# Optimization experiments

Hardware: AMD Instinct MI355X
Metric: run time of the kernel (lower is better)

## Reference

```python
import jax, jax.numpy as jnp
import numpy as np

KERNEL = 3

def setup_inputs() -> dict:
    key = jax.random.key(0)
    k1, k2 = jax.random.split(key)
    x = jax.random.normal(k1, (32, 64, 64, 64), dtype=jnp.float32)
    weights = jax.random.normal(k2, (128, 64, KERNEL * KERNEL), dtype=jnp.float32)
    return {"x": x, "weights": weights}

def reference(x, weights):
    # x: (B, C, H, W); weights: (OC, C, k*k) with torch-unfold ordering
    # (channel slowest, kernel row-major) -> reshape to OIHW conv kernel.
    B, C, H, W = x.shape
    OC = weights.shape[0]
    wk = weights.reshape(OC, C, KERNEL, KERNEL)
    # stride-1, dilation-1, VALID conv == the unfold + per-(oc,c) matmul sum
    y = jax.lax.conv_general_dilated(
        x, wk, window_strides=(1, 1), padding="VALID",
        dimension_numbers=("NCHW", "OIHW", "NCHW"))
    Ho, Wo = y.shape[2], y.shape[3]
    # Faithful replication of the original's layout bug: results are laid out
    # as [oc*B + b] then reinterpreted via view(B, OC, Ho, Wo).
    y = jnp.transpose(y, (1, 0, 2, 3)).reshape(B, OC, Ho, Wo)
    return y
```

## Files before the change

kernel.cpp:

```cpp
#include <hip/hip_runtime.h>


typedef __attribute__((ext_vector_type(8))) short short8;
typedef __attribute__((ext_vector_type(4))) float f32x4;
typedef __attribute__((ext_vector_type(4))) unsigned int uint4v;

__device__ __forceinline__ unsigned short f2bf(float f) {
    unsigned u = __builtin_bit_cast(unsigned, f);
    u = (u + 0x7FFFu + ((u >> 16) & 1u)) >> 16;
    return (unsigned short)u;
}

__device__ __forceinline__ void glds16(const void* g, void* s) {
    __builtin_amdgcn_global_load_lds(
        (const __attribute__((address_space(1))) unsigned int*)g,
        (__attribute__((address_space(3))) unsigned int*)s, 16, 0, 0);
}

__global__ __launch_bounds__(256)
void transpose_x(const float* __restrict__ x, char* __restrict__ xT) {
    __shared__ float tile[64][65];
    const int tid = threadIdx.x;
    const int h = blockIdx.x, b = blockIdx.y;

    #pragma unroll
    for (int i = 0; i < 4; ++i) {
        const int idx = i * 256 + tid;
        const int c = idx >> 4, j = idx & 15;
        const float4 v = *(const float4*)(x + (size_t)(((b * 64 + c) * 64 + h) * 64 + j * 4));
        tile[c][j * 4 + 0] = v.x; tile[c][j * 4 + 1] = v.y;
        tile[c][j * 4 + 2] = v.z; tile[c][j * 4 + 3] = v.w;
    }
    __syncthreads();

    #pragma unroll
    for (int i = 0; i < 2; ++i) {
        const int idx = i * 256 + tid;
        const int col = idx >> 3, q = idx & 7;
        unsigned int wds[4];
        #pragma unroll
        for (int jj = 0; jj < 4; ++jj) {
            const unsigned short lo = f2bf(tile[q * 8 + 2 * jj + 0][col]);
            const unsigned short hi = f2bf(tile[q * 8 + 2 * jj + 1][col]);
            wds[jj] = (unsigned)lo | ((unsigned)hi << 16);
        }
        uint4v v; v[0] = wds[0]; v[1] = wds[1]; v[2] = wds[2]; v[3] = wds[3];
        *(uint4v*)(xT + (size_t)(((b * 64 + h) * 64 + col) * 128) + ((q ^ (col & 7)) * 16)) = v;
    }
}

__global__ __launch_bounds__(256)
void pack_w(const float* __restrict__ w, char* __restrict__ wT) {
    const int id = blockIdx.x * 256 + threadIdx.x;
    const int t = id >> 10;
    const int rem = id & 1023;
    const int oc = rem >> 3, q = rem & 7;
    unsigned int wds[4];
    #pragma unroll
    for (int jj = 0; jj < 4; ++jj) {
        const unsigned short lo = f2bf(w[(size_t)oc * 576 + (q * 8 + 2 * jj + 0) * 9 + t]);
        const unsigned short hi = f2bf(w[(size_t)oc * 576 + (q * 8 + 2 * jj + 1) * 9 + t]);
        wds[jj] = (unsigned)lo | ((unsigned)hi << 16);
    }
    uint4v v; v[0] = wds[0]; v[1] = wds[1]; v[2] = wds[2]; v[3] = wds[3];
    *(uint4v*)(wT + (size_t)(t * 16384 + oc * 128) + ((q ^ (oc & 7)) * 16)) = v;
}

__global__ __launch_bounds__(256, 2)
void quanv_mfma(const char* __restrict__ xT, const char* __restrict__ wT,
                float* __restrict__ out) {
    __shared__ __align__(16) char lds[65536];
    char* sx = lds;
    char* sw = lds + 49152;

    const int tid = threadIdx.x;
    const int lane = tid & 63;
    const int wid = tid >> 6;
    const int hot = blockIdx.x;
    const int b   = blockIdx.y;
    const int ho0 = hot * 4;

    for (int k = wid; k < 48; k += 4) {
        const int r = k >> 3, sub = k & 7;
        int gr = ho0 + r; if (gr > 63) gr = 63;
        glds16(xT + (size_t)((b * 64 + gr) * 8192 + sub * 1024 + lane * 16),
               sx + k * 1024);
    }
    for (int k = wid; k < 16; k += 4)
        glds16(wT + (size_t)(k * 1024 + lane * 16), sw + k * 1024);
    __syncthreads();

    const int l15 = lane & 15;
    const int quad = lane >> 4;
    const int r = wid;
    const int ho = ho0 + r;

    f32x4 acc[8][4];
    #pragma unroll
    for (int mt = 0; mt < 8; ++mt)
        #pragma unroll
        for (int nt = 0; nt < 4; ++nt)
            acc[mt][nt] = (f32x4){0.f, 0.f, 0.f, 0.f};

    #pragma unroll
    for (int tap = 0; tap < 9; ++tap) {
        const int kh = tap / 3, kw = tap % 3;

        uint4v pf[4];
        if (tap < 8) {
            #pragma unroll
            for (int i = 0; i < 4; ++i)
                pf[i] = *(const uint4v*)(wT + (size_t)((tap + 1) * 16384 +
                                                      (wid * 4 + i) * 1024 + lane * 16));
        }

        #pragma unroll
        for (int s = 0; s < 2; ++s) {
            const int q = s * 4 + quad;
            short8 a[8], bf[4];
            const int abase = l15 * 128 + ((q ^ (l15 & 7)) * 16);
            #pragma unroll
            for (int mt = 0; mt < 8; ++mt)
                a[mt] = *(const short8*)(sw + abase + mt * 2048);
            const int cb = kw + l15;
            const int bbase = (r + kh) * 8192 + cb * 128 + ((q ^ (cb & 7)) * 16);
            #pragma unroll
            for (int nt = 0; nt < 4; ++nt)
                bf[nt] = *(const short8*)(sx + bbase + nt * 2048);
            #pragma unroll
            for (int mt = 0; mt < 8; ++mt)
                #pragma unroll
                for (int nt = 0; nt < 4; ++nt)
                    acc[mt][nt] = __builtin_amdgcn_mfma_f32_16x16x32_bf16(
                        a[mt], bf[nt], acc[mt][nt], 0, 0, 0);
        }

        if (tap < 8) {
            __syncthreads();
            #pragma unroll
            for (int i = 0; i < 4; ++i)
                *(uint4v*)(sw + (wid * 4 + i) * 1024 + lane * 16) = pf[i];
            __syncthreads();
        }
    }

    if (ho < 62) {
        #pragma unroll
        for (int mt = 0; mt < 8; ++mt) {
            #pragma unroll
            for (int i = 0; i < 4; ++i) {
                const int oc = mt * 16 + quad * 4 + i;
                float* op = out + ((size_t)(oc * 32 + b) * 62 + ho) * 62;
                #pragma unroll
                for (int nt = 0; nt < 4; ++nt) {
                    const int wo = nt * 16 + l15;
                    if (wo < 62) op[wo] = acc[mt][nt][i];
                }
            }
        }
    }
}

#define CCH   8
#define OC_PT 8
#define ROWS  18
__global__ __launch_bounds__(256, 4)
void quanv_f32(const float* __restrict__ x, const float* __restrict__ w,
               float* __restrict__ out) {
    __shared__ float sx_raw[CCH * ROWS * 64 + 4];
    #define SX(cl, row, col) sx_raw[((cl) * ROWS + (row)) * 64 + (col)]
    const int tid = threadIdx.x;
    const int tx = tid & 15, ty = tid >> 4;
    const int hot = blockIdx.x, ocg = blockIdx.y, b = blockIdx.z;
    const int row0 = hot * 16, ho = row0 + ty, wo0 = tx * 4;
    const float* xb = x + (size_t)b * (64 * 64 * 64);
    const float* wb = w + (size_t)(ocg * OC_PT) * 576;
    float acc[OC_PT][4];
    #pragma unroll
    for (int o = 0; o < OC_PT; ++o)
        #pragma unroll
        for (int q = 0; q < 4; ++q) acc[o][q] = 0.f;
    for (int cc = 0; cc < 64; cc += CCH) {
        __syncthreads();
        #pragma unroll
        for (int j = 0; j < 9; ++j) {
            const int idx = j * 256 + tid;
            const int col4 = idx & 15, rowc = idx >> 4;
            const int row = rowc % ROWS, cl = rowc / ROWS;
            int gr = row0 + row; if (gr > 63) gr = 63;
            *(float4*)(&sx_raw[idx * 4]) =
                *(const float4*)(xb + ((size_t)(cc + cl) * 64 + gr) * 64 + col4 * 4);
        }
        __syncthreads();
        for (int cl = 0; cl < CCH; ++cl) {
            float xv[3][6];
            #pragma unroll
            for (int kh = 0; kh < 3; ++kh)
                #pragma unroll
                for (int j = 0; j < 6; ++j) xv[kh][j] = SX(cl, ty + kh, wo0 + j);
            const float* wc = wb + (size_t)(cc + cl) * 9;
            #pragma unroll
            for (int o = 0; o < OC_PT; ++o) {
                float wv[9];
                #pragma unroll
                for (int t = 0; t < 9; ++t) wv[t] = wc[(size_t)o * 576 + t];
                #pragma unroll
                for (int kh = 0; kh < 3; ++kh)
                    #pragma unroll
                    for (int kw = 0; kw < 3; ++kw) {
                        const float wvv = wv[kh * 3 + kw];
                        #pragma unroll
                        for (int q = 0; q < 4; ++q)
                            acc[o][q] = fmaf(xv[kh][kw + q], wvv, acc[o][q]);
                    }
            }
        }
    }
    if (ho < 62) {
        #pragma unroll
        for (int o = 0; o < OC_PT; ++o) {
            const int oc = ocg * OC_PT + o;
            float* op = out + ((size_t)(oc * 32 + b) * 62 + ho) * 62 + wo0;
            #pragma unroll
            for (int q = 0; q < 4; ++q)
                if (wo0 + q < 62) op[q] = acc[o][q];
        }
    }
    #undef SX
}

extern "C" void kernel_launch(void* const* d_in, const int* in_sizes, int n_in,
                              void* d_out, int out_size, void* d_ws, size_t ws_size,
                              hipStream_t stream) {
    const float* x = (const float*)d_in[0];
    const float* w = (const float*)d_in[1];
    float* out = (float*)d_out;

    const size_t XT_BYTES = 16777216;
    const size_t WT_BYTES = 147456;

    if (ws_size >= XT_BYTES + WT_BYTES) {
        char* xT = (char*)d_ws;
        char* wT = (char*)d_ws + XT_BYTES;
        transpose_x<<<dim3(64, 32), 256, 0, stream>>>(x, xT);
        pack_w<<<36, 256, 0, stream>>>(w, wT);
        quanv_mfma<<<dim3(16, 32), 256, 0, stream>>>(xT, wT, out);
    } else {
        quanv_f32<<<dim3(4, 16, 32), 256, 0, stream>>>(x, w, out);
    }
}
```

Baseline: 115.1 us.

## Switch conv MFMA kernel to 32x32x16 tiles with weights read from global

Replaces the 16x16x32 bf16 MFMA main kernel with one using 32x32x16 MFMA, so each wave computes 128 oc by 64 wo with fewer, larger instructions. Weight fragments are now loaded directly from global memory (L2/L1-cached) per tap instead of being staged in LDS, which removes the per-tap double __syncthreads and the LDS weight buffer. Input rows get a padded row stride to cut LDS bank conflicts. The trade-off is more global-load latency on the critical path for the weight operands, and larger accumulator fragments that raise register pressure.

```diff
diff --git a/kernel.cpp b/kernel.cpp
--- a/kernel.cpp
+++ b/kernel.cpp
@@ -2,7 +2,7 @@
 
 
 typedef __attribute__((ext_vector_type(8))) short short8;
-typedef __attribute__((ext_vector_type(4))) float f32x4;
+typedef __attribute__((ext_vector_type(16))) float f32x16;
 typedef __attribute__((ext_vector_type(4))) unsigned int uint4v;
 
 __device__ __forceinline__ unsigned short f2bf(float f) {
@@ -66,96 +66,84 @@
     *(uint4v*)(wT + (size_t)(t * 16384 + oc * 128) + ((q ^ (oc & 7)) * 16)) = v;
 }
 
+#define ROWSTRIDE 8448
+
 __global__ __launch_bounds__(256, 2)
-void quanv_mfma(const char* __restrict__ xT, const char* __restrict__ wT,
-                float* __restrict__ out) {
-    __shared__ __align__(16) char lds[65536];
-    char* sx = lds;
-    char* sw = lds + 49152;
-
-    const int tid = threadIdx.x;
+void quanv_mfma32(const char* __restrict__ xT, const char* __restrict__ wT,
+                  float* __restrict__ out) {
+    __shared__ __align__(16) char sx[6 * ROWSTRIDE];
+
+    const int tid  = threadIdx.x;
     const int lane = tid & 63;
-    const int wid = tid >> 6;
-    const int hot = blockIdx.x;
-    const int b   = blockIdx.y;
-    const int ho0 = hot * 4;
+    const int wid  = tid >> 6;
+    const int hot  = blockIdx.x;
+    const int b    = blockIdx.y;
+    const int ho0  = hot * 4;
 
     for (int k = wid; k < 48; k += 4) {
         const int r = k >> 3, sub = k & 7;
         int gr = ho0 + r; if (gr > 63) gr = 63;
         glds16(xT + (size_t)((b * 64 + gr) * 8192 + sub * 1024 + lane * 16),
-               sx + k * 1024);
-    }
-    for (int k = wid; k < 16; k += 4)
-        glds16(wT + (size_t)(k * 1024 + lane * 16), sw + k * 1024);
+               sx + r * ROWSTRIDE + sub * 1024);
+    }
     __syncthreads();
 
-    const int l15 = lane & 15;
-    const int quad = lane >> 4;
-    const int r = wid;
-    const int ho = ho0 + r;
-
-    f32x4 acc[8][4];
-    #pragma unroll
-    for (int mt = 0; mt < 8; ++mt)
-        #pragma unroll
-        for (int nt = 0; nt < 4; ++nt)
-            acc[mt][nt] = (f32x4){0.f, 0.f, 0.f, 0.f};
+    const int l31 = lane & 31;
+    const int hi  = lane >> 5;
+    const int ho  = ho0 + wid;
+
+    int voff[4];
+    #pragma unroll
+    for (int kc = 0; kc < 4; ++kc)
+        voff[kc] = l31 * 128 + (((kc * 2 + hi) ^ (l31 & 7)) * 16);
+
+    f32x16 acc[4][2];
+    #pragma unroll
+    for (int mt = 0; mt < 4; ++mt)
+        #pragma unroll
+        for (int nt = 0; nt < 2; ++nt)
+            #pragma unroll
+            for (int e = 0; e < 16; ++e) acc[mt][nt][e] = 0.f;
 
     #pragma unroll
     for (int tap = 0; tap < 9; ++tap) {
         const int kh = tap / 3, kw = tap % 3;
-
-        uint4v pf[4];
-        if (tap < 8) {
-            #pragma unroll
-            for (int i = 0; i < 4; ++i)
-                pf[i] = *(const uint4v*)(wT + (size_t)((tap + 1) * 16384 +
-                                                      (wid * 4 + i) * 1024 + lane * 16));
-        }
-
-        #pragma unroll
-        for (int s = 0; s < 2; ++s) {
-            const int q = s * 4 + quad;
-            short8 a[8], bf[4];
-            const int abase = l15 * 128 + ((q ^ (l15 & 7)) * 16);
-            #pragma unroll
-            for (int mt = 0; mt < 8; ++mt)
-                a[mt] = *(const short8*)(sw + abase + mt * 2048);
-            const int cb = kw + l15;
-            const int bbase = (r + kh) * 8192 + cb * 128 + ((q ^ (cb & 7)) * 16);
-            #pragma unroll
-            for (int nt = 0; nt < 4; ++nt)
-                bf[nt] = *(const short8*)(sx + bbase + nt * 2048);
-            #pragma unroll
-            for (int mt = 0; mt < 8; ++mt)
-                #pragma unroll
-                for (int nt = 0; nt < 4; ++nt)
-                    acc[mt][nt] = __builtin_amdgcn_mfma_f32_16x16x32_bf16(
-                        a[mt], bf[nt], acc[mt][nt], 0, 0, 0);
-        }
-
-        if (tap < 8) {
-            __syncthreads();
-            #pragma unroll
-            for (int i = 0; i < 4; ++i)
-                *(uint4v*)(sw + (wid * 4 + i) * 1024 + lane * 16) = pf[i];
-            __syncthreads();
+        const char* wtap = wT + (size_t)tap * 16384;
+
+        short8 a[4][4];
+        #pragma unroll
+        for (int kc = 0; kc < 4; ++kc)
+            #pragma unroll
+            for (int mt = 0; mt < 4; ++mt)
+                a[kc][mt] = *(const short8*)(wtap + mt * 4096 + voff[kc]);
+
+        const int colswz = (kw + l31) & 7;
+        const int bbase  = (wid + kh) * ROWSTRIDE + (kw + l31) * 128;
+        #pragma unroll
+        for (int kc = 0; kc < 4; ++kc) {
+            short8 bf[2];
+            #pragma unroll
+            for (int nt = 0; nt < 2; ++nt)
+                bf[nt] = *(const short8*)(sx + bbase + nt * 4096 +
+                                          (((kc * 2 + hi) ^ colswz) * 16));
+            #pragma unroll
+            for (int mt = 0; mt < 4; ++mt)
+                #pragma unroll
+                for (int nt = 0; nt < 2; ++nt)
+                    acc[mt][nt] = __builtin_amdgcn_mfma_f32_32x32x16_bf16(
+                        a[kc][mt], bf[nt], acc[mt][nt], 0, 0, 0);
         }
     }
 
     if (ho < 62) {
         #pragma unroll
-        for (int mt = 0; mt < 8; ++mt) {
-            #pragma unroll
-            for (int i = 0; i < 4; ++i) {
-                const int oc = mt * 16 + quad * 4 + i;
+        for (int mt = 0; mt < 4; ++mt) {
+            #pragma unroll
+            for (int r = 0; r < 16; ++r) {
+                const int oc = mt * 32 + (r & 3) + 8 * (r >> 2) + 4 * hi;
                 float* op = out + ((size_t)(oc * 32 + b) * 62 + ho) * 62;
-                #pragma unroll
-                for (int nt = 0; nt < 4; ++nt) {
-                    const int wo = nt * 16 + l15;
-                    if (wo < 62) op[wo] = acc[mt][nt][i];
-                }
+                op[l31] = acc[mt][0][r];
+                if (l31 < 30) op[32 + l31] = acc[mt][1][r];
             }
         }
     }
@@ -244,7 +232,7 @@
         char* wT = (char*)d_ws + XT_BYTES;
         transpose_x<<<dim3(64, 32), 256, 0, stream>>>(x, xT);
         pack_w<<<36, 256, 0, stream>>>(w, wT);
-        quanv_mfma<<<dim3(16, 32), 256, 0, stream>>>(xT, wT, out);
+        quanv_mfma32<<<dim3(16, 32), 256, 0, stream>>>(xT, wT, out);
     } else {
         quanv_f32<<<dim3(4, 16, 32), 256, 0, stream>>>(x, w, out);
     }
```

Result: slower. 122.5 us (+6.4%).
